# Kernel tuning notes

Measured on AMD Instinct MI355X. Metric: run time of the kernel, lower is better.

## Reference

```python
import jax, jax.numpy as jnp
import numpy as np
import math

B, S, E = 32, 4096, 1024
H, D = 16, 64          # n_head, model_dim (per-head qk dim)
NV = E // H            # per-head value dim

def setup_inputs() -> dict:
    key = jax.random.key(0)
    ks = jax.random.split(key, 8)
    sc = 1.0 / math.sqrt(E)
    return {
        "seq1": jax.random.normal(ks[0], (B, 1, E), jnp.float32),
        "seq2": jax.random.normal(ks[1], (B, S, E), jnp.float32),
        "mask": jax.random.randint(ks[2], (B, 1, 1, S), 0, 2, jnp.int32),
        "Wq": jax.random.normal(ks[3], (E, H * D), jnp.float32) * sc,
        "bq": jnp.zeros((H * D,), jnp.float32),
        "Wk": jax.random.normal(ks[4], (E, H * D), jnp.float32) * sc,
        "bk": jnp.zeros((H * D,), jnp.float32),
        "Wv": jax.random.normal(ks[5], (E, E), jnp.float32) * sc,
        "bv": jnp.zeros((E,), jnp.float32),
    }

def reference(seq1, seq2, mask, Wq, bq, Wk, bk, Wv, bv):
    batch, seq_num, dim = seq2.shape
    q = seq1 @ Wq + bq                                   # [B,1,H*D]
    k = seq2 @ Wk + bk                                   # [B,S,H*D]
    v = seq2 @ Wv + bv                                   # [B,S,E]
    q = q.reshape(batch, 1, H, D).transpose(0, 2, 1, 3)      # [B,H,1,D]
    k = k.reshape(batch, seq_num, H, D).transpose(0, 2, 1, 3) # [B,H,S,D]
    v = v.reshape(batch, seq_num, H, NV).transpose(0, 2, 1, 3)# [B,H,S,NV]
    score = jnp.einsum('bhqd,bhkd->bhqk', q, k) / math.sqrt(D)  # [B,H,1,S]
    score = jnp.where(mask == 0, jnp.float32(-1e9), score)
    attn = jax.nn.softmax(score, axis=-1)
    out = jnp.einsum('bhqk,bhkn->bhqn', attn, v)             # [B,H,1,NV]
    return out.transpose(0, 2, 1, 3).reshape(batch, 1, dim)   # [B,1,E]
```

## Files before the change

kernel.cpp:

```cpp
#include <hip/hip_runtime.h>

#define B_  32
#define S_  4096
#define E_  1024
#define H_  16
#define D_  64
#define NV_ 64
#define HD_ 1024

typedef unsigned short ushort_t;
typedef __attribute__((ext_vector_type(8))) short  short8;
typedef __attribute__((ext_vector_type(4))) float  floatx4;

__device__ __forceinline__ ushort_t f2b(float f) {
  union { float f; unsigned int u; } v; v.f = f;
  return (ushort_t)((v.u + 0x7FFFu + ((v.u >> 16) & 1u)) >> 16);
}
__device__ __forceinline__ unsigned int pk2(float lo, float hi) {
  union { float f; unsigned int u; } a, b; a.f = lo; b.f = hi;
  return ((a.u + 0x8000u) >> 16) | ((b.u + 0x8000u) & 0xFFFF0000u);
}

__global__ __launch_bounds__(256) void qr_kernel(
    const float* __restrict__ seq1, const float* __restrict__ Wq,
    const float* __restrict__ bq,   const float* __restrict__ Wk,
    ushort_t* __restrict__ r_bf) {
  __shared__ __align__(16) float qp[4][64];
  __shared__ __align__(16) float qv[64];
  const int b = blockIdx.x / H_, h = blockIdx.x % H_;
  const int t = threadIdx.x;
  const int d = t & 63, quarter = t >> 6;

  {
    const float* s1 = seq1 + (size_t)b * E_;
    const float* wq = Wq + h * D_ + d;
    float sum = 0.f;
    const int e0 = quarter * 256;
    for (int e = e0; e < e0 + 256; ++e)
      sum += s1[e] * wq[(size_t)e * HD_];
    qp[quarter][d] = sum;
  }
  __syncthreads();
  if (t < 64) qv[t] = qp[0][t] + qp[1][t] + qp[2][t] + qp[3][t] + bq[h * D_ + t];
  __syncthreads();

  for (int i = 0; i < 4; ++i) {
    const int e = t + 256 * i;
    const float* wk = Wk + (size_t)e * HD_ + h * D_;
    float rs = 0.f;
#pragma unroll
    for (int g = 0; g < 16; ++g) {
      const float4 w4 = *(const float4*)(wk + g * 4);
      rs += w4.x * qv[g * 4 + 0] + w4.y * qv[g * 4 + 1] +
            w4.z * qv[g * 4 + 2] + w4.w * qv[g * 4 + 3];
    }
    r_bf[((size_t)b * H_ + h) * E_ + e] = f2b(rs * 0.125f);
  }
}

__global__ __launch_bounds__(256) void attn_kernel(
    const float* __restrict__ seq2, const int* __restrict__ mask,
    const ushort_t* __restrict__ r_bf, float* __restrict__ cpart,
    float* __restrict__ mlpart, int NC, int TPC) {
  __shared__ __align__(16) ushort_t rS[16][1032];
  __shared__ __align__(16) ushort_t xS[16][1032];
  __shared__ __align__(16) float scp[4][16][17];
  __shared__ __align__(16) float Pt[16][16];
  __shared__ __align__(16) float mS[16], lS[16], alphaS[16];

  const int b = blockIdx.y, chunk = blockIdx.x;
  const int t = threadIdx.x;
  const int lane = t & 63, w = t >> 6;
  const int s0 = chunk * (TPC * 16);
  const int e0 = t * 4;

  {
    const uint4* src = (const uint4*)(r_bf + (size_t)b * H_ * E_);
#pragma unroll
    for (int i = 0; i < 8; ++i) {
      const int f = t + 256 * i;
      *(uint4*)&rS[f >> 7][(f & 127) * 8] = src[f];
    }
  }
  if (t < 16) { mS[t] = -3e38f; lS[t] = 0.f; }

  float c[16][4];
#pragma unroll
  for (int h = 0; h < 16; ++h)
#pragma unroll
    for (int j = 0; j < 4; ++j) c[h][j] = 0.f;

  for (int it = 0; it < TPC; ++it) {
    const int st = s0 + it * 16;
    __syncthreads();
    {
      const float4* src = (const float4*)(seq2 + ((size_t)b * S_ + st) * E_);
#pragma unroll
      for (int i = 0; i < 16; ++i) {
        const int f = t + 256 * i;
        const float4 v = src[f];
        *(uint2*)&xS[f >> 8][(f & 255) * 4] =
            make_uint2(pk2(v.x, v.y), pk2(v.z, v.w));
      }
    }
    __syncthreads();

    {
      const int m = lane & 15, q = lane >> 4;
      floatx4 acc = {0.f, 0.f, 0.f, 0.f};
#pragma unroll
      for (int kk = 0; kk < 8; ++kk) {
        const int kb = w * 256 + kk * 32 + q * 8;
        short8 av  = *(const short8*)&xS[m][kb];
        short8 bvf = *(const short8*)&rS[m][kb];
        acc = __builtin_amdgcn_mfma_f32_16x16x32_bf16(av, bvf, acc, 0, 0, 0);
      }
#pragma unroll
      for (int j = 0; j < 4; ++j)
        scp[w][q * 4 + j][m] = acc[j];
    }
    __syncthreads();

    if (w == 0) {
      const int h = lane & 15, sg = lane >> 4;
      float sc[4];
#pragma unroll
      for (int j = 0; j < 4; ++j) {
        const int s = sg * 4 + j;
        float v = scp[0][s][h] + scp[1][s][h] + scp[2][s][h] + scp[3][s][h];
        if (mask[(size_t)b * S_ + st + s] == 0) v = -1e9f;
        sc[j] = v;
      }
      float tm = fmaxf(fmaxf(sc[0], sc[1]), fmaxf(sc[2], sc[3]));
      tm = fmaxf(tm, __shfl_xor(tm, 16));
      tm = fmaxf(tm, __shfl_xor(tm, 32));
      const float mo = mS[h];
      const float nm = fmaxf(mo, tm);
      const float al = __expf(mo - nm);
      float ps = 0.f;
#pragma unroll
      for (int j = 0; j < 4; ++j) {
        const float p = __expf(sc[j] - nm);
        Pt[sg * 4 + j][h] = p;
        ps += p;
      }
      ps += __shfl_xor(ps, 16);
      ps += __shfl_xor(ps, 32);
      if (lane < 16) { mS[h] = nm; alphaS[h] = al; lS[h] = lS[h] * al + ps; }
    }
    __syncthreads();

    {
#pragma unroll
      for (int h = 0; h < 16; ++h) {
        const float a = alphaS[h];
        c[h][0] *= a; c[h][1] *= a; c[h][2] *= a; c[h][3] *= a;
      }
#pragma unroll
      for (int s = 0; s < 16; ++s) {
        union { uint2 v; ushort_t u[4]; } xr;
        xr.v = *(const uint2*)&xS[s][e0];
        union { unsigned int i; float f; } cv;
        cv.i = (unsigned int)xr.u[0] << 16; const float x0 = cv.f;
        cv.i = (unsigned int)xr.u[1] << 16; const float x1 = cv.f;
        cv.i = (unsigned int)xr.u[2] << 16; const float x2 = cv.f;
        cv.i = (unsigned int)xr.u[3] << 16; const float x3 = cv.f;
        float p[16];
        *(float4*)&p[0]  = *(const float4*)&Pt[s][0];
        *(float4*)&p[4]  = *(const float4*)&Pt[s][4];
        *(float4*)&p[8]  = *(const float4*)&Pt[s][8];
        *(float4*)&p[12] = *(const float4*)&Pt[s][12];
#pragma unroll
        for (int h = 0; h < 16; ++h) {
          c[h][0] += p[h] * x0; c[h][1] += p[h] * x1;
          c[h][2] += p[h] * x2; c[h][3] += p[h] * x3;
        }
      }
    }
  }

  const size_t base = ((size_t)b * NC + chunk) * H_ * E_;
#pragma unroll
  for (int h = 0; h < 16; ++h)
    *(float4*)&cpart[base + (size_t)h * E_ + e0] =
        make_float4(c[h][0], c[h][1], c[h][2], c[h][3]);
  if (t < 16) {
    mlpart[(((size_t)b * NC + chunk) * H_ + t) * 2 + 0] = mS[t];
    mlpart[(((size_t)b * NC + chunk) * H_ + t) * 2 + 1] = lS[t];
  }
}

__global__ __launch_bounds__(256) void combine_kernel(
    const float* __restrict__ cpart, const float* __restrict__ mlpart,
    const float* __restrict__ Wv, const float* __restrict__ bvp,
    float* __restrict__ out, int NC) {
  __shared__ __align__(16) float wS[64];
  __shared__ __align__(16) float cnS[1024];
  __shared__ __align__(16) float vp[4][64];
  __shared__ float invLS;
  const int b = blockIdx.x / H_, h = blockIdx.x % H_;
  const int t = threadIdx.x;

  if (t < 64) {
    float m_i = -3e38f, l_i = 0.f;
    if (t < NC) {
      const size_t mi = (((size_t)b * NC + t) * H_ + h) * 2;
      m_i = mlpart[mi]; l_i = mlpart[mi + 1];
    }
    float M = m_i;
#pragma unroll
    for (int dlt = 1; dlt < 64; dlt <<= 1) M = fmaxf(M, __shfl_xor(M, dlt));
    const float wi = (t < NC) ? __expf(m_i - M) : 0.f;
    float Lp = l_i * wi;
#pragma unroll
    for (int dlt = 1; dlt < 64; dlt <<= 1) Lp += __shfl_xor(Lp, dlt);
    if (t < NC) wS[t] = wi;
    if (t == 0) invLS = 1.f / Lp;
  }
  __syncthreads();

  {
    const int e0 = t * 4;
    float a0 = 0.f, a1 = 0.f, a2 = 0.f, a3 = 0.f;
    for (int i = 0; i < NC; ++i) {
      const float wi = wS[i];
      const float4 v =
          *(const float4*)&cpart[(((size_t)b * NC + i) * H_ + h) * E_ + e0];
      a0 += wi * v.x; a1 += wi * v.y; a2 += wi * v.z; a3 += wi * v.w;
    }
    const float inv = invLS;
    *(float4*)&cnS[e0] = make_float4(a0 * inv, a1 * inv, a2 * inv, a3 * inv);
  }
  __syncthreads();

  {
    const int n = t & 63, part = t >> 6;
    const float* wv = Wv + h * NV_ + n;
    float sum = 0.f;
    const int eb = part * 256;
    for (int e = eb; e < eb + 256; ++e)
      sum += cnS[e] * wv[(size_t)e * E_];
    vp[part][n] = sum;
  }
  __syncthreads();
  if (t < 64) {
    const float o = vp[0][t] + vp[1][t] + vp[2][t] + vp[3][t] + bvp[h * NV_ + t];
    out[(size_t)b * E_ + h * NV_ + t] = o;
  }
}

extern "C" void kernel_launch(void* const* d_in, const int* in_sizes, int n_in,
                              void* d_out, int out_size, void* d_ws, size_t ws_size,
                              hipStream_t stream) {
  const float* seq1 = (const float*)d_in[0];
  const float* seq2 = (const float*)d_in[1];
  const int*   mask = (const int*)d_in[2];
  const float* Wq   = (const float*)d_in[3];
  const float* bq   = (const float*)d_in[4];
  const float* Wk   = (const float*)d_in[5];
  const float* Wv   = (const float*)d_in[7];
  const float* bv   = (const float*)d_in[8];
  float* out = (float*)d_out;

  const size_t rbytes = (size_t)B_ * H_ * E_ * 2;
  int NC = 16;
  while (NC > 1) {
    const size_t need = rbytes + (size_t)B_ * NC * H_ * E_ * 4
                               + (size_t)B_ * NC * H_ * 2 * 4;
    if (need <= ws_size) break;
    NC >>= 1;
  }
  const int TPC = (S_ / NC) / 16;
  ushort_t* r_bf = (ushort_t*)d_ws;
  float* cpart   = (float*)((char*)d_ws + rbytes);
  float* mlpart  = (float*)((char*)d_ws + rbytes + (size_t)B_ * NC * H_ * E_ * 4);

  qr_kernel<<<dim3(B_ * H_), dim3(256), 0, stream>>>(seq1, Wq, bq, Wk, r_bf);
  attn_kernel<<<dim3(NC, B_), dim3(256), 0, stream>>>(seq2, mask, r_bf, cpart,
                                                      mlpart, NC, TPC);
  combine_kernel<<<dim3(B_ * H_), dim3(256), 0, stream>>>(cpart, mlpart, Wv, bv,
                                                          out, NC);
}
```

Measured before the change: 798.8 us.

## Double-buffer seq2 tiles with register prefetch and keep r in registers

The attention kernel now prefetches the next 16-row seq2 tile into registers while computing on the current tile, writing it to a second shared-memory buffer after the PV accumulation. This removes one barrier per iteration and is meant to overlap global-load latency with compute. The r operand is held in registers instead of shared memory, and the mask is loaded as an int4 ahead of use. It also sets a launch bound of 2 blocks per CU and raises the chunk count to 32 for more parallelism, at the cost of higher register pressure (64 floats of accumulators plus 16 float4 prefetch registers) and larger partial buffers for the combine kernel.

```diff
diff --git a/kernel.cpp b/kernel.cpp
--- a/kernel.cpp
+++ b/kernel.cpp
@@ -58,12 +58,11 @@
   }
 }
 
-__global__ __launch_bounds__(256) void attn_kernel(
+__global__ __launch_bounds__(256, 2) void attn_kernel(
     const float* __restrict__ seq2, const int* __restrict__ mask,
     const ushort_t* __restrict__ r_bf, float* __restrict__ cpart,
     float* __restrict__ mlpart, int NC, int TPC) {
-  __shared__ __align__(16) ushort_t rS[16][1032];
-  __shared__ __align__(16) ushort_t xS[16][1032];
+  __shared__ __align__(16) ushort_t xS[2][16][1032];
   __shared__ __align__(16) float scp[4][16][17];
   __shared__ __align__(16) float Pt[16][16];
   __shared__ __align__(16) float mS[16], lS[16], alphaS[16];
@@ -71,16 +70,15 @@
   const int b = blockIdx.y, chunk = blockIdx.x;
   const int t = threadIdx.x;
   const int lane = t & 63, w = t >> 6;
+  const int m = lane & 15, q = lane >> 4;
   const int s0 = chunk * (TPC * 16);
   const int e0 = t * 4;
 
-  {
-    const uint4* src = (const uint4*)(r_bf + (size_t)b * H_ * E_);
-#pragma unroll
-    for (int i = 0; i < 8; ++i) {
-      const int f = t + 256 * i;
-      *(uint4*)&rS[f >> 7][(f & 127) * 8] = src[f];
-    }
+  short8 rf[8];
+  {
+    const ushort_t* rb = r_bf + ((size_t)b * H_ + m) * E_ + w * 256 + q * 8;
+#pragma unroll
+    for (int kk = 0; kk < 8; ++kk) rf[kk] = *(const short8*)(rb + kk * 32);
   }
   if (t < 16) { mS[t] = -3e38f; lS[t] = 0.f; }
 
@@ -90,30 +88,39 @@
 #pragma unroll
     for (int j = 0; j < 4; ++j) c[h][j] = 0.f;
 
+  float4 xr[16];
+  {
+    const float4* src = (const float4*)(seq2 + ((size_t)b * S_ + s0) * E_);
+#pragma unroll
+    for (int i = 0; i < 16; ++i) xr[i] = src[t + 256 * i];
+#pragma unroll
+    for (int i = 0; i < 16; ++i)
+      *(uint2*)&xS[0][i][t * 4] =
+          make_uint2(pk2(xr[i].x, xr[i].y), pk2(xr[i].z, xr[i].w));
+  }
+  __syncthreads();
+
   for (int it = 0; it < TPC; ++it) {
+    const int p = it & 1;
     const int st = s0 + it * 16;
-    __syncthreads();
+    const bool more = (it + 1 < TPC);
+
+    if (more) {
+      const float4* src =
+          (const float4*)(seq2 + ((size_t)b * S_ + st + 16) * E_);
+#pragma unroll
+      for (int i = 0; i < 16; ++i) xr[i] = src[t + 256 * i];
+    }
+    int4 mk;
+    if (w == 0) mk = *(const int4*)&mask[(size_t)b * S_ + st + q * 4];
+
     {
-      const float4* src = (const float4*)(seq2 + ((size_t)b * S_ + st) * E_);
-#pragma unroll
-      for (int i = 0; i < 16; ++i) {
-        const int f = t + 256 * i;
-        const float4 v = src[f];
-        *(uint2*)&xS[f >> 8][(f & 255) * 4] =
-            make_uint2(pk2(v.x, v.y), pk2(v.z, v.w));
-      }
-    }
-    __syncthreads();
-
-    {
-      const int m = lane & 15, q = lane >> 4;
       floatx4 acc = {0.f, 0.f, 0.f, 0.f};
 #pragma unroll
       for (int kk = 0; kk < 8; ++kk) {
         const int kb = w * 256 + kk * 32 + q * 8;
-        short8 av  = *(const short8*)&xS[m][kb];
-        short8 bvf = *(const short8*)&rS[m][kb];
-        acc = __builtin_amdgcn_mfma_f32_16x16x32_bf16(av, bvf, acc, 0, 0, 0);
+        short8 av = *(const short8*)&xS[p][m][kb];
+        acc = __builtin_amdgcn_mfma_f32_16x16x32_bf16(av, rf[kk], acc, 0, 0, 0);
       }
 #pragma unroll
       for (int j = 0; j < 4; ++j)
@@ -122,13 +129,14 @@
     __syncthreads();
 
     if (w == 0) {
-      const int h = lane & 15, sg = lane >> 4;
+      const int h = m, sg = q;
+      const int mki[4] = {mk.x, mk.y, mk.z, mk.w};
       float sc[4];
 #pragma unroll
       for (int j = 0; j < 4; ++j) {
         const int s = sg * 4 + j;
         float v = scp[0][s][h] + scp[1][s][h] + scp[2][s][h] + scp[3][s][h];
-        if (mask[(size_t)b * S_ + st + s] == 0) v = -1e9f;
+        if (mki[j] == 0) v = -1e9f;
         sc[j] = v;
       }
       float tm = fmaxf(fmaxf(sc[0], sc[1]), fmaxf(sc[2], sc[3]));
@@ -140,9 +148,9 @@
       float ps = 0.f;
 #pragma unroll
       for (int j = 0; j < 4; ++j) {
-        const float p = __expf(sc[j] - nm);
-        Pt[sg * 4 + j][h] = p;
-        ps += p;
+        const float pj = __expf(sc[j] - nm);
+        Pt[sg * 4 + j][h] = pj;
+        ps += pj;
       }
       ps += __shfl_xor(ps, 16);
       ps += __shfl_xor(ps, 32);
@@ -158,25 +166,33 @@
       }
 #pragma unroll
       for (int s = 0; s < 16; ++s) {
-        union { uint2 v; ushort_t u[4]; } xr;
-        xr.v = *(const uint2*)&xS[s][e0];
+        union { uint2 v; ushort_t u[4]; } xv;
+        xv.v = *(const uint2*)&xS[p][s][e0];
         union { unsigned int i; float f; } cv;
-        cv.i = (unsigned int)xr.u[0] << 16; const float x0 = cv.f;
-        cv.i = (unsigned int)xr.u[1] << 16; const float x1 = cv.f;
-        cv.i = (unsigned int)xr.u[2] << 16; const float x2 = cv.f;
-        cv.i = (unsigned int)xr.u[3] << 16; const float x3 = cv.f;
-        float p[16];
-        *(float4*)&p[0]  = *(const float4*)&Pt[s][0];
-        *(float4*)&p[4]  = *(const float4*)&Pt[s][4];
-        *(float4*)&p[8]  = *(const float4*)&Pt[s][8];
-        *(float4*)&p[12] = *(const float4*)&Pt[s][12];
+        cv.i = (unsigned int)xv.u[0] << 16; const float x0 = cv.f;
+        cv.i = (unsigned int)xv.u[1] << 16; const float x1 = cv.f;
+        cv.i = (unsigned int)xv.u[2] << 16; const float x2 = cv.f;
+        cv.i = (unsigned int)xv.u[3] << 16; const float x3 = cv.f;
+        float pv[16];
+        *(float4*)&pv[0]  = *(const float4*)&Pt[s][0];
+        *(float4*)&pv[4]  = *(const float4*)&Pt[s][4];
+        *(float4*)&pv[8]  = *(const float4*)&Pt[s][8];
+        *(float4*)&pv[12] = *(const float4*)&Pt[s][12];
 #pragma unroll
         for (int h = 0; h < 16; ++h) {
-          c[h][0] += p[h] * x0; c[h][1] += p[h] * x1;
-          c[h][2] += p[h] * x2; c[h][3] += p[h] * x3;
+          c[h][0] += pv[h] * x0; c[h][1] += pv[h] * x1;
+          c[h][2] += pv[h] * x2; c[h][3] += pv[h] * x3;
         }
       }
     }
+
+    if (more) {
+#pragma unroll
+      for (int i = 0; i < 16; ++i)
+        *(uint2*)&xS[p ^ 1][i][t * 4] =
+            make_uint2(pk2(xr[i].x, xr[i].y), pk2(xr[i].z, xr[i].w));
+    }
+    __syncthreads();
   }
 
   const size_t base = ((size_t)b * NC + chunk) * H_ * E_;
@@ -263,7 +279,7 @@
   float* out = (float*)d_out;
 
   const size_t rbytes = (size_t)B_ * H_ * E_ * 2;
-  int NC = 16;
+  int NC = 32;
   while (NC > 1) {
     const size_t need = rbytes + (size_t)B_ * NC * H_ * E_ * 4
                                + (size_t)B_ * NC * H_ * 2 * 4;
```

New measurement: 1.732 ms. 2.17x slower.
